# Kernel tuning notes

Measured on AMD Instinct MI355X. Metric: run time of the kernel, lower is better.

Reference implementation:

```python
import jax, jax.numpy as jnp
import numpy as np

N, C, T, V = 64, 64, 256, 25
O, R = 64, 8  # out_channels, rel_channels = in_channels // 8


def _conv1x1(x, W, b):
    # x: [N,C,T,V], W: [O,C], b: [O] -> [N,O,T,V]
    return jnp.einsum('oc,nctv->notv', W, x) + b[None, :, None, None]


def setup_inputs() -> dict:
    key = jax.random.key(0)
    ks = jax.random.split(key, 16)
    s = 0.05
    return {
        'x': jax.random.normal(ks[0], (N, C, T, V), jnp.float32),
        'A': jax.random.normal(ks[1], (V, V), jnp.float32),
        'W1': jax.random.normal(ks[2], (R, C), jnp.float32) * s,
        'b1': jnp.zeros((R,), jnp.float32),
        'W2': jax.random.normal(ks[3], (R, C), jnp.float32) * s,
        'b2': jnp.zeros((R,), jnp.float32),
        'W3': jax.random.normal(ks[4], (O, C), jnp.float32) * s,
        'b3': jnp.zeros((O,), jnp.float32),
        'W4': jax.random.normal(ks[5], (O, R), jnp.float32) * s,
        'b4': jnp.zeros((O,), jnp.float32),
        'W5': jax.random.normal(ks[6], (R, C), jnp.float32) * s,
        'b5': jnp.zeros((R,), jnp.float32),
        'w6': jax.random.normal(ks[7], (), jnp.float32),
        'b6': jnp.zeros((), jnp.float32),
        'w7': jax.random.normal(ks[8], (), jnp.float32),
        'b7': jnp.zeros((), jnp.float32),
    }


def reference(x, A, W1, b1, W2, b2, W3, b3, W4, b4, W5, b5, w6, b6, w7, b7):
    alpha = 1.0
    beta = 1.0
    # branch projections
    x1m = _conv1x1(x, W1, b1).mean(axis=2)          # [N,R,V]
    x2m = _conv1x1(x, W2, b2).mean(axis=2)          # [N,R,V]
    x3 = _conv1x1(x, W3, b3)                        # [N,O,T,V]
    # topology refinement: tanh of pairwise differences -> [N,R,V,V]
    d = jnp.tanh(x1m[:, :, :, None] - x2m[:, :, None, :])
    # per-channel attention (vectorized over the rel_channels loop).
    # q@k^T = 25 * (w6*m_u+b6)*(w7*m_v+b7); /sqrt(25) -> factor 5.
    m = _conv1x1(x, W5, b5).mean(axis=2)            # [N,R,V]
    q = w6 * m + b6
    k = w7 * m + b7
    att = 5.0 * q[:, :, :, None] * k[:, :, None, :]  # [N,R,V,V]
    res = jnp.tanh(jax.nn.softmax(att, axis=-1))     # [N,R,V,V]
    # conv4 lifts rel_channels -> out_channels on the VxV maps
    proj = lambda t: jnp.einsum('or,nruv->nouv', W4, t) + b4[None, :, None, None]
    adj = proj(d) * alpha + A[None, None, :, :] + proj(res) * beta  # [N,O,V,V]
    # aggregate: einsum('ncuv,nctv->nctu')
    return jnp.einsum('nouv,notv->notu', adj, x3)    # [N,O,T,V]
```

## Files before the change

kernel.cpp:

```cpp
#include <hip/hip_runtime.h>


#define N_ 64
#define C_ 64
#define T_ 256
#define V_ 25
#define O_ 64
#define R_ 8

#define TV_ (T_*V_)
#define XM_FLOATS (N_*C_*V_)
#define ADJ_STRIDE 28
#define ADJ_ROW (V_*ADJ_STRIDE)

__global__ __launch_bounds__(256) void k1_mean(const float* __restrict__ x,
                                               float* __restrict__ xm) {
  __shared__ float xl[TV_];
  __shared__ float red[4][V_];
  const int tid = threadIdx.x;
  const size_t base = (size_t)blockIdx.x * TV_;
  const float4* xg = reinterpret_cast<const float4*>(x + base);
  for (int i = tid; i < TV_/4; i += 256) {
    float4 v = xg[i];
    float* dst = &xl[4*i];
    dst[0]=v.x; dst[1]=v.y; dst[2]=v.z; dst[3]=v.w;
  }
  __syncthreads();
  float s[V_];
  #pragma unroll
  for (int v = 0; v < V_; ++v) s[v] = xl[tid*V_ + v];
  #pragma unroll
  for (int v = 0; v < V_; ++v) {
    #pragma unroll
    for (int off = 32; off >= 1; off >>= 1) s[v] += __shfl_xor(s[v], off);
  }
  const int lane = tid & 63, w = tid >> 6;
  if (lane == 0) {
    #pragma unroll
    for (int v = 0; v < V_; ++v) red[w][v] = s[v];
  }
  __syncthreads();
  if (tid < V_) {
    float t = red[0][tid] + red[1][tid] + red[2][tid] + red[3][tid];
    xm[(size_t)blockIdx.x * V_ + tid] = t * (1.0f / T_);
  }
}

__global__ __launch_bounds__(256) void k2_adj(
    const float* __restrict__ xm, const float* __restrict__ A,
    const float* __restrict__ W1, const float* __restrict__ b1,
    const float* __restrict__ W2, const float* __restrict__ b2,
    const float* __restrict__ W4, const float* __restrict__ b4,
    const float* __restrict__ W5, const float* __restrict__ b5,
    const float* __restrict__ w6p, const float* __restrict__ b6p,
    const float* __restrict__ w7p, const float* __restrict__ b7p,
    float* __restrict__ adjP) {
  __shared__ float xmL[C_ * V_];
  __shared__ float p1[R_ * V_];
  __shared__ float p2[R_ * V_];
  __shared__ float pm[R_ * V_];
  __shared__ float dres[R_][V_][V_];
  const int n = blockIdx.x, tid = threadIdx.x;

  for (int i = tid; i < C_ * V_; i += 256) xmL[i] = xm[(size_t)n * C_ * V_ + i];
  __syncthreads();

  for (int i = tid; i < 3 * R_ * V_; i += 256) {
    const int which = i / (R_ * V_), rem = i % (R_ * V_);
    const int r = rem / V_, v = rem % V_;
    const float* W = (which == 0) ? W1 : (which == 1) ? W2 : W5;
    const float* b = (which == 0) ? b1 : (which == 1) ? b2 : b5;
    float s = b[r];
    for (int c = 0; c < C_; ++c) s += W[r * C_ + c] * xmL[c * V_ + v];
    float* P = (which == 0) ? p1 : (which == 1) ? p2 : pm;
    P[rem] = s;
  }
  __syncthreads();

  if (tid < R_ * V_) {
    const int r = tid / V_, u = tid % V_;
    const float w6 = w6p[0], b6 = b6p[0], w7 = w7p[0], b7 = b7p[0];
    const float qu = w6 * pm[r * V_ + u] + b6;
    float e[V_];
    float mx = -INFINITY;
    #pragma unroll
    for (int v = 0; v < V_; ++v) {
      float a = 5.0f * qu * (w7 * pm[r * V_ + v] + b7);
      e[v] = a;
      mx = fmaxf(mx, a);
    }
    float ssum = 0.f;
    #pragma unroll
    for (int v = 0; v < V_; ++v) { float ev = expf(e[v] - mx); e[v] = ev; ssum += ev; }
    const float inv = 1.0f / ssum;
    const float p1u = p1[r * V_ + u];
    #pragma unroll
    for (int v = 0; v < V_; ++v) {
      float res = tanhf(e[v] * inv);
      float dv  = tanhf(p1u - p2[r * V_ + v]);
      dres[r][u][v] = dv + res;
    }
  }
  __syncthreads();

  for (int i = tid; i < O_ * V_; i += 256) {
    const int o = i / V_, u = i % V_;
    const float b4o2 = 2.0f * b4[o];
    float w4r[R_];
    #pragma unroll
    for (int r = 0; r < R_; ++r) w4r[r] = W4[o * R_ + r];
    float* dst = adjP + (size_t)(n * O_ + o) * ADJ_ROW + (size_t)u * ADJ_STRIDE;
    #pragma unroll
    for (int v = 0; v < V_; ++v) {
      float s = b4o2 + A[u * V_ + v];
      #pragma unroll
      for (int r = 0; r < R_; ++r) s += w4r[r] * dres[r][u][v];
      dst[v] = s;
    }
  }
}

#define TT 8
#define OSTEP 4
__global__ __launch_bounds__(256, 4) void kF(const float* __restrict__ x,
                                             const float* __restrict__ W3,
                                             const float* __restrict__ b3,
                                             const float* __restrict__ adjP,
                                             float* __restrict__ out) {
  __shared__ float x3L[OSTEP][TT][32];
  __shared__ __align__(16) float adjL[OSTEP][ADJ_ROW];
  const int tid = threadIdx.x;
  const int t  = tid >> 5;
  const int vp = tid & 31;
  const int n  = blockIdx.y;
  const int t0 = blockIdx.x * TT;
  const size_t nbase = (size_t)n * C_ * TV_;
  const int vclamp = (vp < V_) ? vp : (V_ - 1);
  const int col = (t0 + t) * V_ + vclamp;

  float xv[C_];
  #pragma unroll
  for (int c = 0; c < C_; ++c) xv[c] = x[nbase + (size_t)c * TV_ + col];

  const float* adjN = adjP + (size_t)n * O_ * ADJ_ROW;
  const bool active_u = (vp < V_);
  const int ui = active_u ? vp : 0;

  for (int op = 0; op < O_; op += OSTEP) {
    float4 a[OSTEP];
    if (tid < ADJ_ROW / 4) {
      #pragma unroll
      for (int k = 0; k < OSTEP; ++k)
        a[k] = reinterpret_cast<const float4*>(adjN + (size_t)(op + k) * ADJ_ROW)[tid];
    }
    #pragma unroll
    for (int k = 0; k < OSTEP; ++k) {
      const float* wr = W3 + (op + k) * C_;
      float s0 = 0.f, s1 = 0.f, s2 = 0.f, s3 = 0.f;
      #pragma unroll
      for (int c = 0; c < C_; c += 4) {
        s0 += wr[c+0] * xv[c+0];
        s1 += wr[c+1] * xv[c+1];
        s2 += wr[c+2] * xv[c+2];
        s3 += wr[c+3] * xv[c+3];
      }
      x3L[k][t][vp] = (s0 + s1) + (s2 + s3) + b3[op + k];
    }
    if (tid < ADJ_ROW / 4) {
      #pragma unroll
      for (int k = 0; k < OSTEP; ++k)
        reinterpret_cast<float4*>(&adjL[k][0])[tid] = a[k];
    }
    __syncthreads();
    #pragma unroll
    for (int k = 0; k < OSTEP; ++k) {
      const float* ar = &adjL[k][ui * ADJ_STRIDE];
      const float* xr = &x3L[k][t][0];
      float acc = 0.f;
      #pragma unroll
      for (int j = 0; j < 6; ++j) {
        float4 av = *reinterpret_cast<const float4*>(ar + 4 * j);
        float4 xw = *reinterpret_cast<const float4*>(xr + 4 * j);
        acc += av.x * xw.x + av.y * xw.y + av.z * xw.z + av.w * xw.w;
      }
      acc += ar[24] * xr[24];
      if (active_u)
        out[nbase + (size_t)(op + k) * TV_ + (size_t)(t0 + t) * V_ + vp] = acc;
    }
    __syncthreads();
  }
}

extern "C" void kernel_launch(void* const* d_in, const int* in_sizes, int n_in,
                              void* d_out, int out_size, void* d_ws, size_t ws_size,
                              hipStream_t stream) {
  const float* x  = (const float*)d_in[0];
  const float* A  = (const float*)d_in[1];
  const float* W1 = (const float*)d_in[2];
  const float* b1 = (const float*)d_in[3];
  const float* W2 = (const float*)d_in[4];
  const float* b2 = (const float*)d_in[5];
  const float* W3 = (const float*)d_in[6];
  const float* b3 = (const float*)d_in[7];
  const float* W4 = (const float*)d_in[8];
  const float* b4 = (const float*)d_in[9];
  const float* W5 = (const float*)d_in[10];
  const float* b5 = (const float*)d_in[11];
  const float* w6 = (const float*)d_in[12];
  const float* b6 = (const float*)d_in[13];
  const float* w7 = (const float*)d_in[14];
  const float* b7 = (const float*)d_in[15];
  float* out  = (float*)d_out;
  float* xm   = (float*)d_ws;
  float* adjP = xm + XM_FLOATS;

  k1_mean<<<dim3(N_ * C_), 256, 0, stream>>>(x, xm);
  k2_adj<<<dim3(N_), 256, 0, stream>>>(xm, A, W1, b1, W2, b2, W4, b4, W5, b5,
                                       w6, b6, w7, b7, adjP);
  kF<<<dim3(T_ / TT, N_), 256, 0, stream>>>(x, W3, b3, adjP, out);
}
```

Measured before the change: 445.6 us.

## Fuse mean and adjacency kernels via last-block atomic; restructure conv3 and coalesce stores

Merges the per-channel T-mean kernel and the per-sample adjacency kernel into one launch. The last block to finish for each sample, detected with an atomic counter, computes that sample's adjacency, and a small kernel zeroes the counters beforehand. The final kernel now stages a transposed W3 in shared memory and computes all 64 conv3 outputs per thread up front, instead of recomputing dot products from registers per output group. Output tiles are staged in shared memory so global stores are coalesced float4 writes. The trade-offs are an extra launch, higher register pressure from the 64-entry accumulator array, and extra barriers per output group.

```diff
diff --git a/kernel.cpp b/kernel.cpp
--- a/kernel.cpp
+++ b/kernel.cpp
@@ -12,42 +12,18 @@
 #define XM_FLOATS (N_*C_*V_)
 #define ADJ_STRIDE 28
 #define ADJ_ROW (V_*ADJ_STRIDE)
-
-__global__ __launch_bounds__(256) void k1_mean(const float* __restrict__ x,
-                                               float* __restrict__ xm) {
-  __shared__ float xl[TV_];
-  __shared__ float red[4][V_];
-  const int tid = threadIdx.x;
-  const size_t base = (size_t)blockIdx.x * TV_;
-  const float4* xg = reinterpret_cast<const float4*>(x + base);
-  for (int i = tid; i < TV_/4; i += 256) {
-    float4 v = xg[i];
-    float* dst = &xl[4*i];
-    dst[0]=v.x; dst[1]=v.y; dst[2]=v.z; dst[3]=v.w;
-  }
-  __syncthreads();
-  float s[V_];
-  #pragma unroll
-  for (int v = 0; v < V_; ++v) s[v] = xl[tid*V_ + v];
-  #pragma unroll
-  for (int v = 0; v < V_; ++v) {
-    #pragma unroll
-    for (int off = 32; off >= 1; off >>= 1) s[v] += __shfl_xor(s[v], off);
-  }
-  const int lane = tid & 63, w = tid >> 6;
-  if (lane == 0) {
-    #pragma unroll
-    for (int v = 0; v < V_; ++v) red[w][v] = s[v];
-  }
-  __syncthreads();
-  if (tid < V_) {
-    float t = red[0][tid] + red[1][tid] + red[2][tid] + red[3][tid];
-    xm[(size_t)blockIdx.x * V_ + tid] = t * (1.0f / T_);
-  }
-}
-
-__global__ __launch_bounds__(256) void k2_adj(
-    const float* __restrict__ xm, const float* __restrict__ A,
+#define RV_ (R_*V_)
+#define TT 8
+#define OSTEP 4
+
+__global__ void kZero(unsigned int* __restrict__ cnt) {
+  if (threadIdx.x < N_) cnt[threadIdx.x] = 0u;
+}
+
+__global__ __launch_bounds__(256) void kPre(
+    const float* __restrict__ x, float* __restrict__ xm,
+    unsigned int* __restrict__ cnt,
+    const float* __restrict__ A,
     const float* __restrict__ W1, const float* __restrict__ b1,
     const float* __restrict__ W2, const float* __restrict__ b2,
     const float* __restrict__ W4, const float* __restrict__ b4,
@@ -55,37 +31,79 @@
     const float* __restrict__ w6p, const float* __restrict__ b6p,
     const float* __restrict__ w7p, const float* __restrict__ b7p,
     float* __restrict__ adjP) {
-  __shared__ float xmL[C_ * V_];
-  __shared__ float p1[R_ * V_];
-  __shared__ float p2[R_ * V_];
-  __shared__ float pm[R_ * V_];
-  __shared__ float dres[R_][V_][V_];
-  const int n = blockIdx.x, tid = threadIdx.x;
-
-  for (int i = tid; i < C_ * V_; i += 256) xmL[i] = xm[(size_t)n * C_ * V_ + i];
-  __syncthreads();
-
-  for (int i = tid; i < 3 * R_ * V_; i += 256) {
-    const int which = i / (R_ * V_), rem = i % (R_ * V_);
+  __shared__ union {
+    struct { float xl[TV_]; float red[4][V_]; } p1;
+    struct { float xmL[C_*V_]; float q1[RV_]; float q2[RV_]; float qm[RV_];
+             float dres[R_][V_][V_]; } p2;
+  } u;
+  __shared__ int winner;
+  const int tid = threadIdx.x;
+  const int bid = blockIdx.x;
+  const int n = bid >> 6;
+
+  {
+    const size_t base = (size_t)bid * TV_;
+    const float4* xg = reinterpret_cast<const float4*>(x + base);
+    for (int i = tid; i < TV_/4; i += 256) {
+      float4 v = xg[i];
+      float* dst = &u.p1.xl[4*i];
+      dst[0]=v.x; dst[1]=v.y; dst[2]=v.z; dst[3]=v.w;
+    }
+    __syncthreads();
+    float s[V_];
+    #pragma unroll
+    for (int v = 0; v < V_; ++v) s[v] = u.p1.xl[tid*V_ + v];
+    #pragma unroll
+    for (int v = 0; v < V_; ++v) {
+      #pragma unroll
+      for (int off = 32; off >= 1; off >>= 1) s[v] += __shfl_xor(s[v], off);
+    }
+    const int lane = tid & 63, wv = tid >> 6;
+    if (lane == 0) {
+      #pragma unroll
+      for (int v = 0; v < V_; ++v) u.p1.red[wv][v] = s[v];
+    }
+    __syncthreads();
+    if (tid < V_) {
+      float t = u.p1.red[0][tid]+u.p1.red[1][tid]+u.p1.red[2][tid]+u.p1.red[3][tid];
+      xm[(size_t)bid * V_ + tid] = t * (1.0f / T_);
+    }
+  }
+
+  __threadfence();
+  __syncthreads();
+  if (tid == 0) {
+    unsigned int old = atomicAdd(&cnt[n], 1u);
+    winner = (old == C_ - 1u) ? 1 : 0;
+  }
+  __syncthreads();
+  if (!winner) return;
+  __threadfence();
+
+  for (int i = tid; i < C_ * V_; i += 256) u.p2.xmL[i] = xm[(size_t)n * C_ * V_ + i];
+  __syncthreads();
+
+  for (int i = tid; i < 3 * RV_; i += 256) {
+    const int which = i / RV_, rem = i % RV_;
     const int r = rem / V_, v = rem % V_;
     const float* W = (which == 0) ? W1 : (which == 1) ? W2 : W5;
     const float* b = (which == 0) ? b1 : (which == 1) ? b2 : b5;
     float s = b[r];
-    for (int c = 0; c < C_; ++c) s += W[r * C_ + c] * xmL[c * V_ + v];
-    float* P = (which == 0) ? p1 : (which == 1) ? p2 : pm;
+    for (int c = 0; c < C_; ++c) s += W[r * C_ + c] * u.p2.xmL[c * V_ + v];
+    float* P = (which == 0) ? u.p2.q1 : (which == 1) ? u.p2.q2 : u.p2.qm;
     P[rem] = s;
   }
   __syncthreads();
 
-  if (tid < R_ * V_) {
-    const int r = tid / V_, u = tid % V_;
+  if (tid < RV_) {
+    const int r = tid / V_, uu = tid % V_;
     const float w6 = w6p[0], b6 = b6p[0], w7 = w7p[0], b7 = b7p[0];
-    const float qu = w6 * pm[r * V_ + u] + b6;
+    const float qu = w6 * u.p2.qm[r * V_ + uu] + b6;
     float e[V_];
     float mx = -INFINITY;
     #pragma unroll
     for (int v = 0; v < V_; ++v) {
-      float a = 5.0f * qu * (w7 * pm[r * V_ + v] + b7);
+      float a = 5.0f * qu * (w7 * u.p2.qm[r * V_ + v] + b7);
       e[v] = a;
       mx = fmaxf(mx, a);
     }
@@ -93,42 +111,41 @@
     #pragma unroll
     for (int v = 0; v < V_; ++v) { float ev = expf(e[v] - mx); e[v] = ev; ssum += ev; }
     const float inv = 1.0f / ssum;
-    const float p1u = p1[r * V_ + u];
+    const float q1u = u.p2.q1[r * V_ + uu];
     #pragma unroll
     for (int v = 0; v < V_; ++v) {
       float res = tanhf(e[v] * inv);
-      float dv  = tanhf(p1u - p2[r * V_ + v]);
-      dres[r][u][v] = dv + res;
+      float dv  = tanhf(q1u - u.p2.q2[r * V_ + v]);
+      u.p2.dres[r][uu][v] = dv + res;
     }
   }
   __syncthreads();
 
   for (int i = tid; i < O_ * V_; i += 256) {
-    const int o = i / V_, u = i % V_;
+    const int o = i / V_, uu = i % V_;
     const float b4o2 = 2.0f * b4[o];
     float w4r[R_];
     #pragma unroll
     for (int r = 0; r < R_; ++r) w4r[r] = W4[o * R_ + r];
-    float* dst = adjP + (size_t)(n * O_ + o) * ADJ_ROW + (size_t)u * ADJ_STRIDE;
-    #pragma unroll
-    for (int v = 0; v < V_; ++v) {
-      float s = b4o2 + A[u * V_ + v];
-      #pragma unroll
-      for (int r = 0; r < R_; ++r) s += w4r[r] * dres[r][u][v];
+    float* dst = adjP + (size_t)(n * O_ + o) * ADJ_ROW + (size_t)uu * ADJ_STRIDE;
+    #pragma unroll
+    for (int v = 0; v < V_; ++v) {
+      float s = b4o2 + A[uu * V_ + v];
+      #pragma unroll
+      for (int r = 0; r < R_; ++r) s += w4r[r] * u.p2.dres[r][uu][v];
       dst[v] = s;
     }
   }
 }
 
-#define TT 8
-#define OSTEP 4
-__global__ __launch_bounds__(256, 4) void kF(const float* __restrict__ x,
-                                             const float* __restrict__ W3,
-                                             const float* __restrict__ b3,
-                                             const float* __restrict__ adjP,
-                                             float* __restrict__ out) {
+__global__ __launch_bounds__(256, 4) void kF2(
+    const float* __restrict__ x, const float* __restrict__ W3,
+    const float* __restrict__ b3, const float* __restrict__ adjP,
+    float* __restrict__ out) {
+  __shared__ __align__(16) float W3T[C_ * O_];
+  __shared__ __align__(16) float adjL[OSTEP][ADJ_ROW];
   __shared__ float x3L[OSTEP][TT][32];
-  __shared__ __align__(16) float adjL[OSTEP][ADJ_ROW];
+  __shared__ float oL[OSTEP][TT][26];
   const int tid = threadIdx.x;
   const int t  = tid >> 5;
   const int vp = tid & 31;
@@ -137,55 +154,71 @@
   const size_t nbase = (size_t)n * C_ * TV_;
   const int vclamp = (vp < V_) ? vp : (V_ - 1);
   const int col = (t0 + t) * V_ + vclamp;
-
-  float xv[C_];
+  const bool active_u = (vp < V_);
+
+  for (int i = tid; i < C_ * O_; i += 256) {
+    const int o = i >> 6, c = i & 63;
+    W3T[c * O_ + o] = W3[i];
+  }
+  __syncthreads();
+
+  float acc[O_];
   #pragma unroll
-  for (int c = 0; c < C_; ++c) xv[c] = x[nbase + (size_t)c * TV_ + col];
+  for (int o = 0; o < O_; ++o) acc[o] = 0.f;
+  #pragma unroll 4
+  for (int c = 0; c < C_; ++c) {
+    const float xc = x[nbase + (size_t)c * TV_ + col];
+    const float4* wrow = reinterpret_cast<const float4*>(&W3T[c * O_]);
+    #pragma unroll
+    for (int j = 0; j < O_/4; ++j) {
+      float4 wv = wrow[j];
+      acc[4*j+0] += wv.x * xc;
+      acc[4*j+1] += wv.y * xc;
+      acc[4*j+2] += wv.z * xc;
+      acc[4*j+3] += wv.w * xc;
+    }
+  }
 
   const float* adjN = adjP + (size_t)n * O_ * ADJ_ROW;
-  const bool active_u = (vp < V_);
-  const int ui = active_u ? vp : 0;
-
+  float* outN = out + nbase;
+
+  #pragma unroll
   for (int op = 0; op < O_; op += OSTEP) {
-    float4 a[OSTEP];
     if (tid < ADJ_ROW / 4) {
       #pragma unroll
-      for (int k = 0; k < OSTEP; ++k)
-        a[k] = reinterpret_cast<const float4*>(adjN + (size_t)(op + k) * ADJ_ROW)[tid];
-    }
+      for (int k = 0; k < OSTEP; ++k) {
+        float4 a = reinterpret_cast<const float4*>(adjN + (size_t)(op + k) * ADJ_ROW)[tid];
+        reinterpret_cast<float4*>(&adjL[k][0])[tid] = a;
+      }
+    }
+    #pragma unroll
+    for (int k = 0; k < OSTEP; ++k)
+      x3L[k][t][vp] = acc[op + k] + b3[op + k];
+    __syncthreads();
     #pragma unroll
     for (int k = 0; k < OSTEP; ++k) {
-      const float* wr = W3 + (op + k) * C_;
-      float s0 = 0.f, s1 = 0.f, s2 = 0.f, s3 = 0.f;
-      #pragma unroll
-      for (int c = 0; c < C_; c += 4) {
-        s0 += wr[c+0] * xv[c+0];
-        s1 += wr[c+1] * xv[c+1];
-        s2 += wr[c+2] * xv[c+2];
-        s3 += wr[c+3] * xv[c+3];
-      }
-      x3L[k][t][vp] = (s0 + s1) + (s2 + s3) + b3[op + k];
-    }
-    if (tid < ADJ_ROW / 4) {
-      #pragma unroll
-      for (int k = 0; k < OSTEP; ++k)
-        reinterpret_cast<float4*>(&adjL[k][0])[tid] = a[k];
-    }
-    __syncthreads();
-    #pragma unroll
-    for (int k = 0; k < OSTEP; ++k) {
-      const float* ar = &adjL[k][ui * ADJ_STRIDE];
+      const float* ar = &adjL[k][(active_u ? vp : 0) * ADJ_STRIDE];
       const float* xr = &x3L[k][t][0];
-      float acc = 0.f;
+      float s = 0.f;
       #pragma unroll
       for (int j = 0; j < 6; ++j) {
         float4 av = *reinterpret_cast<const float4*>(ar + 4 * j);
         float4 xw = *reinterpret_cast<const float4*>(xr + 4 * j);
-        acc += av.x * xw.x + av.y * xw.y + av.z * xw.z + av.w * xw.w;
+        s += av.x * xw.x + av.y * xw.y + av.z * xw.z + av.w * xw.w;
       }
-      acc += ar[24] * xr[24];
-      if (active_u)
-        out[nbase + (size_t)(op + k) * TV_ + (size_t)(t0 + t) * V_ + vp] = acc;
+      s += ar[24] * xr[24];
+      if (active_u) oL[k][t][vp] = s;
+    }
+    __syncthreads();
+    if (tid < OSTEP * 50) {
+      const int p = tid / 50, rem = tid - p * 50;
+      const int e = rem * 4;
+      float4 vv;
+      vv.x = oL[p][(e    ) / V_][(e    ) % V_];
+      vv.y = oL[p][(e + 1) / V_][(e + 1) % V_];
+      vv.z = oL[p][(e + 2) / V_][(e + 2) % V_];
+      vv.w = oL[p][(e + 3) / V_][(e + 3) % V_];
+      reinterpret_cast<float4*>(outN + (size_t)(op + p) * TV_ + (size_t)t0 * V_)[rem] = vv;
     }
     __syncthreads();
   }
@@ -210,12 +243,14 @@
   const float* b6 = (const float*)d_in[13];
   const float* w7 = (const float*)d_in[14];
   const float* b7 = (const float*)d_in[15];
-  float* out  = (float*)d_out;
-  float* xm   = (float*)d_ws;
-  float* adjP = xm + XM_FLOATS;
-
-  k1_mean<<<dim3(N_ * C_), 256, 0, stream>>>(x, xm);
-  k2_adj<<<dim3(N_), 256, 0, stream>>>(xm, A, W1, b1, W2, b2, W4, b4, W5, b5,
-                                       w6, b6, w7, b7, adjP);
-  kF<<<dim3(T_ / TT, N_), 256, 0, stream>>>(x, W3, b3, adjP, out);
-}
+  float* out = (float*)d_out;
+
+  float* xm = (float*)d_ws;
+  unsigned int* cnt = (unsigned int*)((char*)d_ws + XM_FLOATS * 4);
+  float* adjP = (float*)((char*)d_ws + XM_FLOATS * 4 + 256);
+
+  kZero<<<dim3(1), 64, 0, stream>>>(cnt);
+  kPre<<<dim3(N_ * C_), 256, 0, stream>>>(x, xm, cnt, A, W1, b1, W2, b2,
+                                          W4, b4, W5, b5, w6, b6, w7, b7, adjP);
+  kF2<<<dim3(T_ / TT, N_), 256, 0, stream>>>(x, W3, b3, adjP, out);
+}
```

After: 1.271 ms. 185% more time.

## Compute all x3 outputs upfront with shared-memory W3 and stage output stores

Applied to the files above, without the earlier changes.

The fused kernel now transposes W3 into shared memory once per block. Each thread keeps all 64 conv3 outputs in registers, built by streaming x one channel at a time, instead of holding 64 x values and redoing dot products with global W3 reads. Outputs for each group of four channels are staged in shared memory and written as coalesced float4 stores rather than scalar stores with 25 of 32 lanes active. The cost is a 64-float accumulator array that raises register pressure under a 4-blocks-per-SM launch bound, plus an extra barrier per output group.

```diff
diff --git a/kernel.cpp b/kernel.cpp
--- a/kernel.cpp
+++ b/kernel.cpp
@@ -12,6 +12,9 @@
 #define XM_FLOATS (N_*C_*V_)
 #define ADJ_STRIDE 28
 #define ADJ_ROW (V_*ADJ_STRIDE)
+#define RV_ (R_*V_)
+#define TT 8
+#define OSTEP 4
 
 __global__ __launch_bounds__(256) void k1_mean(const float* __restrict__ x,
                                                float* __restrict__ xm) {
@@ -56,17 +59,17 @@
     const float* __restrict__ w7p, const float* __restrict__ b7p,
     float* __restrict__ adjP) {
   __shared__ float xmL[C_ * V_];
-  __shared__ float p1[R_ * V_];
-  __shared__ float p2[R_ * V_];
-  __shared__ float pm[R_ * V_];
+  __shared__ float p1[RV_];
+  __shared__ float p2[RV_];
+  __shared__ float pm[RV_];
   __shared__ float dres[R_][V_][V_];
   const int n = blockIdx.x, tid = threadIdx.x;
 
   for (int i = tid; i < C_ * V_; i += 256) xmL[i] = xm[(size_t)n * C_ * V_ + i];
   __syncthreads();
 
-  for (int i = tid; i < 3 * R_ * V_; i += 256) {
-    const int which = i / (R_ * V_), rem = i % (R_ * V_);
+  for (int i = tid; i < 3 * RV_; i += 256) {
+    const int which = i / RV_, rem = i % RV_;
     const int r = rem / V_, v = rem % V_;
     const float* W = (which == 0) ? W1 : (which == 1) ? W2 : W5;
     const float* b = (which == 0) ? b1 : (which == 1) ? b2 : b5;
@@ -77,7 +80,7 @@
   }
   __syncthreads();
 
-  if (tid < R_ * V_) {
+  if (tid < RV_) {
     const int r = tid / V_, u = tid % V_;
     const float w6 = w6p[0], b6 = b6p[0], w7 = w7p[0], b7 = b7p[0];
     const float qu = w6 * pm[r * V_ + u] + b6;
@@ -120,15 +123,14 @@
   }
 }
 
-#define TT 8
-#define OSTEP 4
-__global__ __launch_bounds__(256, 4) void kF(const float* __restrict__ x,
-                                             const float* __restrict__ W3,
-                                             const float* __restrict__ b3,
-                                             const float* __restrict__ adjP,
-                                             float* __restrict__ out) {
+__global__ __launch_bounds__(256, 4) void kF2(
+    const float* __restrict__ x, const float* __restrict__ W3,
+    const float* __restrict__ b3, const float* __restrict__ adjP,
+    float* __restrict__ out) {
+  __shared__ __align__(16) float W3T[C_ * O_];
+  __shared__ __align__(16) float adjL[OSTEP][ADJ_ROW];
   __shared__ float x3L[OSTEP][TT][32];
-  __shared__ __align__(16) float adjL[OSTEP][ADJ_ROW];
+  __shared__ float oL[OSTEP][TT][26];
   const int tid = threadIdx.x;
   const int t  = tid >> 5;
   const int vp = tid & 31;
@@ -137,55 +139,71 @@
   const size_t nbase = (size_t)n * C_ * TV_;
   const int vclamp = (vp < V_) ? vp : (V_ - 1);
   const int col = (t0 + t) * V_ + vclamp;
-
-  float xv[C_];
-  #pragma unroll
-  for (int c = 0; c < C_; ++c) xv[c] = x[nbase + (size_t)c * TV_ + col];
+  const bool active_u = (vp < V_);
+
+  for (int i = tid; i < C_ * O_; i += 256) {
+    const int o = i >> 6, c = i & 63;
+    W3T[c * O_ + o] = W3[i];
+  }
+  __syncthreads();
+
+  float acc[O_];
+  #pragma unroll
+  for (int o = 0; o < O_; ++o) acc[o] = 0.f;
+  #pragma unroll 4
+  for (int c = 0; c < C_; ++c) {
+    const float xc = x[nbase + (size_t)c * TV_ + col];
+    const float4* wrow = reinterpret_cast<const float4*>(&W3T[c * O_]);
+    #pragma unroll
+    for (int j = 0; j < O_/4; ++j) {
+      float4 wv = wrow[j];
+      acc[4*j+0] += wv.x * xc;
+      acc[4*j+1] += wv.y * xc;
+      acc[4*j+2] += wv.z * xc;
+      acc[4*j+3] += wv.w * xc;
+    }
+  }
 
   const float* adjN = adjP + (size_t)n * O_ * ADJ_ROW;
-  const bool active_u = (vp < V_);
-  const int ui = active_u ? vp : 0;
-
+  float* outN = out + nbase;
+
+  #pragma unroll
   for (int op = 0; op < O_; op += OSTEP) {
-    float4 a[OSTEP];
     if (tid < ADJ_ROW / 4) {
       #pragma unroll
-      for (int k = 0; k < OSTEP; ++k)
-        a[k] = reinterpret_cast<const float4*>(adjN + (size_t)(op + k) * ADJ_ROW)[tid];
-    }
+      for (int k = 0; k < OSTEP; ++k) {
+        float4 a = reinterpret_cast<const float4*>(adjN + (size_t)(op + k) * ADJ_ROW)[tid];
+        reinterpret_cast<float4*>(&adjL[k][0])[tid] = a;
+      }
+    }
+    #pragma unroll
+    for (int k = 0; k < OSTEP; ++k)
+      x3L[k][t][vp] = acc[op + k] + b3[op + k];
+    __syncthreads();
     #pragma unroll
     for (int k = 0; k < OSTEP; ++k) {
-      const float* wr = W3 + (op + k) * C_;
-      float s0 = 0.f, s1 = 0.f, s2 = 0.f, s3 = 0.f;
-      #pragma unroll
-      for (int c = 0; c < C_; c += 4) {
-        s0 += wr[c+0] * xv[c+0];
-        s1 += wr[c+1] * xv[c+1];
-        s2 += wr[c+2] * xv[c+2];
-        s3 += wr[c+3] * xv[c+3];
-      }
-      x3L[k][t][vp] = (s0 + s1) + (s2 + s3) + b3[op + k];
-    }
-    if (tid < ADJ_ROW / 4) {
-      #pragma unroll
-      for (int k = 0; k < OSTEP; ++k)
-        reinterpret_cast<float4*>(&adjL[k][0])[tid] = a[k];
-    }
-    __syncthreads();
-    #pragma unroll
-    for (int k = 0; k < OSTEP; ++k) {
-      const float* ar = &adjL[k][ui * ADJ_STRIDE];
+      const float* ar = &adjL[k][(active_u ? vp : 0) * ADJ_STRIDE];
       const float* xr = &x3L[k][t][0];
-      float acc = 0.f;
+      float s = 0.f;
       #pragma unroll
       for (int j = 0; j < 6; ++j) {
         float4 av = *reinterpret_cast<const float4*>(ar + 4 * j);
         float4 xw = *reinterpret_cast<const float4*>(xr + 4 * j);
-        acc += av.x * xw.x + av.y * xw.y + av.z * xw.z + av.w * xw.w;
+        s += av.x * xw.x + av.y * xw.y + av.z * xw.z + av.w * xw.w;
       }
-      acc += ar[24] * xr[24];
-      if (active_u)
-        out[nbase + (size_t)(op + k) * TV_ + (size_t)(t0 + t) * V_ + vp] = acc;
+      s += ar[24] * xr[24];
+      if (active_u) oL[k][t][vp] = s;
+    }
+    __syncthreads();
+    if (tid < OSTEP * 50) {
+      const int p = tid / 50, rem = tid - p * 50;
+      const int e = rem * 4;
+      float4 vv;
+      vv.x = oL[p][(e    ) / V_][(e    ) % V_];
+      vv.y = oL[p][(e + 1) / V_][(e + 1) % V_];
+      vv.z = oL[p][(e + 2) / V_][(e + 2) % V_];
+      vv.w = oL[p][(e + 3) / V_][(e + 3) % V_];
+      reinterpret_cast<float4*>(outN + (size_t)(op + p) * TV_ + (size_t)t0 * V_)[rem] = vv;
     }
     __syncthreads();
   }
@@ -210,12 +228,13 @@
   const float* b6 = (const float*)d_in[13];
   const float* w7 = (const float*)d_in[14];
   const float* b7 = (const float*)d_in[15];
-  float* out  = (float*)d_out;
+  float* out = (float*)d_out;
+
   float* xm   = (float*)d_ws;
   float* adjP = xm + XM_FLOATS;
 
   k1_mean<<<dim3(N_ * C_), 256, 0, stream>>>(x, xm);
   k2_adj<<<dim3(N_), 256, 0, stream>>>(xm, A, W1, b1, W2, b2, W4, b4, W5, b5,
                                        w6, b6, w7, b7, adjP);
-  kF<<<dim3(T_ / TT, N_), 256, 0, stream>>>(x, W3, b3, adjP, out);
-}
+  kF2<<<dim3(T_ / TT, N_), 256, 0, stream>>>(x, W3, b3, adjP, out);
+}
```

Result: slower. 560.2 us (+25.7%).
